# Kernel tuning notes

Measured on AMD Instinct MI355X. Metric: run time of the kernel, lower is better.

The kernel has to match this reference:

```python
import jax, jax.numpy as jnp
from jax import lax
import numpy as np

B, N, D = 32, 256, 4
INF = jnp.float32(1e9)


def cdist(a, b):
    # a: [B,N,D], b: [B,M,D] -> Euclidean cost [B,N,M] (torch.cdist default p=2)
    d = a[:, :, None, :] - b[:, None, :, :]
    return jnp.sqrt(jnp.maximum(jnp.sum(d * d, axis=-1), 0.0))


def hungarian(cost):
    """Exact linear sum assignment (Jonker-Volgenant shortest augmenting path),
    equivalent to scipy.optimize.linear_sum_assignment on a square [n,n] cost.
    Returns col4row[i] = column assigned to row i."""
    n = cost.shape[0]

    def row_step(i, state):  # i in 1..n (1-based row index)
        u, v, p = state  # potentials u:[n+1], v:[n+1]; p[j] = row matched to col j (1-based)
        p = p.at[0].set(i)
        minv = jnp.full(n + 1, INF, dtype=cost.dtype)
        used = jnp.zeros(n + 1, dtype=bool)
        way = jnp.zeros(n + 1, dtype=jnp.int32)
        j0 = jnp.int32(0)

        def cond(c):
            u_, v_, p_, minv_, used_, way_, j0_ = c
            return p_[j0_] != 0

        def body(c):
            u_, v_, p_, minv_, used_, way_, j0_ = c
            used_ = used_.at[j0_].set(True)
            i0 = p_[j0_]
            cur = cost[i0 - 1] - u_[i0] - v_[1:]          # reduced costs for cols 1..n
            cur = jnp.where(used_[1:], INF, cur)
            upd = cur < minv_[1:]
            minv_ = minv_.at[1:].set(jnp.where(upd, cur, minv_[1:]))
            way_ = way_.at[1:].set(jnp.where(upd, j0_, way_[1:]))
            masked = jnp.where(used_[1:], INF, minv_[1:])
            j1 = jnp.argmin(masked).astype(jnp.int32) + 1
            delta = masked[j1 - 1]
            bump = jnp.where(used_, delta, jnp.zeros((), cost.dtype))
            u_ = u_.at[p_].add(bump)                       # u[p[j]] += delta for used j
            v_ = v_ - bump
            minv_ = minv_.at[1:].set(jnp.where(used_[1:], minv_[1:], minv_[1:] - delta))
            return (u_, v_, p_, minv_, used_, way_, j1)

        u, v, p, minv, used, way, j0 = lax.while_loop(cond, body, (u, v, p, minv, used, way, j0))

        def aug_cond(c):
            return c[1] != 0

        def aug_body(c):
            p_, j_ = c
            j1 = way[j_]
            return (p_.at[j_].set(p_[j1]), j1)

        p, _ = lax.while_loop(aug_cond, aug_body, (p, j0))
        return (u, v, p)

    u0 = jnp.zeros(n + 1, dtype=cost.dtype)
    v0 = jnp.zeros(n + 1, dtype=cost.dtype)
    p0 = jnp.zeros(n + 1, dtype=jnp.int32)
    _, _, p = lax.fori_loop(1, n + 1, row_step, (u0, v0, p0))
    # invert: p[j] (1-based row) -> col4row
    col4row = jnp.zeros(n, dtype=jnp.int32).at[p[1:] - 1].set(jnp.arange(n, dtype=jnp.int32))
    return col4row


def setup_inputs() -> dict:
    key = jax.random.key(0)
    k1, k2 = jax.random.split(key)
    pred = jax.random.normal(k1, (B, N, D), dtype=jnp.float32) * 10.0
    gt = jax.random.normal(k2, (B, N, D), dtype=jnp.float32) * 10.0
    return {"pred": pred, "gt": gt}


def reference(pred, gt):
    cost = cdist(pred, gt)                                 # [B,N,N]
    col4row = jax.vmap(hungarian)(cost)                    # [B,N] int32
    matched = jnp.take_along_axis(cost, col4row[:, :, None].astype(jnp.int32), axis=2)[:, :, 0]
    total_cost = matched.sum(axis=-1)                      # [B]
    return col4row, total_cost
```

## Files before the change

kernel.cpp:

```cpp
#include <hip/hip_runtime.h>
#include <math.h>


#define NB   32
#define NN   256
#define ND   4
#define NPT  4
#define INFV 1e9f

#if __has_builtin(__builtin_amdgcn_sqrtf)
__device__ __forceinline__ float fast_sqrtf(float x) { return __builtin_amdgcn_sqrtf(x); }
#else
__device__ __forceinline__ float fast_sqrtf(float x) {
    float r; asm volatile("v_sqrt_f32 %0, %1" : "=v"(r) : "v"(x)); return r;
}
#endif

__device__ __forceinline__ float wave_min_bcast(float x) {
    const int fill = __float_as_int(INFV);
    int a, c;
    a = __builtin_amdgcn_update_dpp(fill, __float_as_int(x), 0x111, 0xF, 0xF, false);
    c = __builtin_amdgcn_update_dpp(fill, __float_as_int(x), 0x112, 0xF, 0xF, false);
    x = fminf(x, fminf(__int_as_float(a), __int_as_float(c)));
    a = __builtin_amdgcn_update_dpp(fill, __float_as_int(x), 0x113, 0xF, 0xF, false);
    c = __builtin_amdgcn_update_dpp(fill, __float_as_int(x), 0x116, 0xF, 0xF, false);
    x = fminf(x, fminf(__int_as_float(a), __int_as_float(c)));
    a = __builtin_amdgcn_update_dpp(fill, __float_as_int(x), 0x117, 0xF, 0xF, false);
    x = fminf(x, __int_as_float(a));
    a = __builtin_amdgcn_update_dpp(fill, __float_as_int(x), 0x142, 0xF, 0xF, false);
    x = fminf(x, __int_as_float(a));
    a = __builtin_amdgcn_update_dpp(fill, __float_as_int(x), 0x143, 0xF, 0xF, false);
    x = fminf(x, __int_as_float(a));
    return __int_as_float(__builtin_amdgcn_readlane(__float_as_int(x), 63));
}

__device__ __forceinline__ float readlane_f(float v, int lane) {
    return __int_as_float(__builtin_amdgcn_readlane(__float_as_int(v), lane));
}
__device__ __forceinline__ int readlane_i(int v, int lane) {
    return __builtin_amdgcn_readlane(v, lane);
}
__device__ __forceinline__ float sel4f(float a0, float a1, float a2, float a3, int kk) {
    float u0 = (kk & 1) ? a1 : a0;
    float u1 = (kk & 1) ? a3 : a2;
    return (kk & 2) ? u1 : u0;
}
__device__ __forceinline__ int sel4i(int a0, int a1, int a2, int a3, int kk) {
    int u0 = (kk & 1) ? a1 : a0;
    int u1 = (kk & 1) ? a3 : a2;
    return (kk & 2) ? u1 : u0;
}

__global__ __launch_bounds__(64) void hungarian_kernel(
    const float* __restrict__ pred, const float* __restrict__ gt,
    float* __restrict__ out)
{
#pragma clang fp contract(off)
    const int b    = blockIdx.x;
    const int lane = threadIdx.x;

    const float* pb = pred + (size_t)b * NN * ND;
    const float* gb = gt   + (size_t)b * NN * ND;

    __shared__ int claimed[NN];

    float gx[NPT], gy[NPT], gz[NPT], gw[NPT];
    float qx[NPT], qy[NPT], qz[NPT], qw[NPT];
    #pragma unroll
    for (int k = 0; k < NPT; ++k) {
        float4 gv = ((const float4*)gb)[4 * lane + k];
        gx[k] = gv.x; gy[k] = gv.y; gz[k] = gv.z; gw[k] = gv.w;
        float4 pv = ((const float4*)pb)[4 * lane + k];
        qx[k] = pv.x; qy[k] = pv.y; qz[k] = pv.z; qw[k] = pv.w;
    }
    float v[NPT], ur[NPT], prx[NPT], pry[NPT], prz[NPT], prw[NPT];
    int pl[NPT];
    #pragma unroll
    for (int k = 0; k < NPT; ++k) {
        v[k] = 0.f; pl[k] = 0; ur[k] = 0.f;
        prx[k] = 0.f; pry[k] = 0.f; prz[k] = 0.f; prw[k] = 0.f;
    }
    const float FINF = __int_as_float(0x7f800000);
    const float NINF = __int_as_float(0xff800000);

    float cmin[NPT];
    int   crow[NPT];
    #pragma unroll
    for (int k = 0; k < NPT; ++k) { cmin[k] = INFV; crow[k] = 0; }
    #pragma unroll 2
    for (int r = 0; r < NN; ++r) {
        const int kkr = r & 3, owr = r >> 2;
        float px = readlane_f(sel4f(qx[0], qx[1], qx[2], qx[3], kkr), owr);
        float py = readlane_f(sel4f(qy[0], qy[1], qy[2], qy[3], kkr), owr);
        float pz = readlane_f(sel4f(qz[0], qz[1], qz[2], qz[3], kkr), owr);
        float pw = readlane_f(sel4f(qw[0], qw[1], qw[2], qw[3], kkr), owr);
        #pragma unroll
        for (int k = 0; k < NPT; ++k) {
            float dx = px - gx[k], dy = py - gy[k];
            float dz = pz - gz[k], dw = pw - gw[k];
            float ss = dx * dx;
            ss = __builtin_fmaf(dy, dy, ss);
            ss = __builtin_fmaf(dz, dz, ss);
            ss = __builtin_fmaf(dw, dw, ss);
            float c = fast_sqrtf(ss);
            bool upd = c < cmin[k];
            crow[k] = upd ? (r + 1) : crow[k];
            cmin[k] = fminf(cmin[k], c);
        }
    }
    #pragma unroll
    for (int k = 0; k < NPT; ++k) claimed[4 * lane + k] = 0x7fffffff;
    __syncthreads();
    #pragma unroll
    for (int k = 0; k < NPT; ++k) atomicMin(&claimed[crow[k] - 1], 4 * lane + k + 1);
    __syncthreads();
    int rm[NPT];
    #pragma unroll
    for (int k = 0; k < NPT; ++k) rm[k] = (claimed[4 * lane + k] != 0x7fffffff);
    #pragma unroll
    for (int k = 0; k < NPT; ++k) {
        v[k]  = cmin[k];
        pl[k] = (claimed[crow[k] - 1] == (4 * lane + k + 1)) ? crow[k] : 0;
    }
    const unsigned long long m0 = __ballot(rm[0]);
    const unsigned long long m1 = __ballot(rm[1]);
    const unsigned long long m2 = __ballot(rm[2]);
    const unsigned long long m3 = __ballot(rm[3]);
    #pragma unroll
    for (int k = 0; k < NPT; ++k) {
        int rr = pl[k];
        if (rr) {
            float4 pv = ((const float4*)pb)[rr - 1];
            prx[k] = pv.x; pry[k] = pv.y; prz[k] = pv.z; prw[k] = pv.w;
        }
    }

    for (int i = 1; i <= NN; ++i) {
        const int im1 = i - 1;
        const unsigned long long mm = (im1 & 2) ? ((im1 & 1) ? m3 : m2)
                                                : ((im1 & 1) ? m1 : m0);
        if ((mm >> (im1 >> 2)) & 1ull) continue;

        const int kki = im1 & 3, owi = im1 >> 2;
        float4 pr0;
        pr0.x = readlane_f(sel4f(qx[0], qx[1], qx[2], qx[3], kki), owi);
        pr0.y = readlane_f(sel4f(qy[0], qy[1], qy[2], qy[3], kki), owi);
        pr0.z = readlane_f(sel4f(qz[0], qz[1], qz[2], qz[3], kki), owi);
        pr0.w = readlane_f(sel4f(qw[0], qw[1], qw[2], qw[3], kki), owi);
        float4 pr = pr0;

        int codes[NPT];
        #pragma unroll
        for (int k = 0; k < NPT; ++k) codes[k] = (4 * lane + k + 1) | (pl[k] << 12);
        float minv[NPT], vm[NPT], ucol[NPT], mcol[NPT];
        int   wayr[NPT];
        #pragma unroll
        for (int k = 0; k < NPT; ++k) {
            minv[k] = INFV; vm[k] = v[k]; ucol[k] = 0.f; mcol[k] = 0.f; wayr[k] = 0;
        }
        float u_i = 0.f;
        int   j1  = 0;
        float ui  = 0.f;
        int   i0n = i;

        for (int it = 0; it < NN + 2; ++it) {
            const int   jm1 = j1 - 1;
            const float bu  = ui - u_i;
            #pragma unroll
            for (int k = 0; k < NPT; ++k) {
                bool hit = (4 * lane + k) == jm1;
                vm[k]   = hit ? NINF : vm[k];
                minv[k] = hit ? FINF : minv[k];
                ucol[k] = hit ? bu   : ucol[k];
                mcol[k] = hit ? u_i  : mcol[k];
            }
            #pragma unroll
            for (int k = 0; k < NPT; ++k) {
                float dx = pr.x - gx[k], dy = pr.y - gy[k];
                float dz = pr.z - gz[k], dw = pr.w - gw[k];
                float ss = dx * dx;
                ss = __builtin_fmaf(dy, dy, ss);
                ss = __builtin_fmaf(dz, dz, ss);
                ss = __builtin_fmaf(dw, dw, ss);
                float cur = (fast_sqrtf(ss) - ui) - vm[k];
                bool upd = cur < minv[k];
                wayr[k] = upd ? j1 : wayr[k];
                minv[k] = fminf(minv[k], cur);
            }
            bool s01 = minv[1] < minv[0];
            float v01 = s01 ? minv[1] : minv[0];
            int   c01 = s01 ? codes[1] : codes[0];
            float u01 = s01 ? ur[1] : ur[0];
            float x01 = s01 ? prx[1] : prx[0];
            float y01 = s01 ? pry[1] : pry[0];
            float z01 = s01 ? prz[1] : prz[0];
            float w01 = s01 ? prw[1] : prw[0];
            bool s23 = minv[3] < minv[2];
            float v23 = s23 ? minv[3] : minv[2];
            int   c23 = s23 ? codes[3] : codes[2];
            float u23 = s23 ? ur[3] : ur[2];
            float x23 = s23 ? prx[3] : prx[2];
            float y23 = s23 ? pry[3] : pry[2];
            float z23 = s23 ? prz[3] : prz[2];
            float w23 = s23 ? prw[3] : prw[2];
            bool sF  = v23 < v01;
            float best       = sF ? v23 : v01;
            int   code_local = sF ? c23 : c01;
            float usel = sF ? u23 : u01;
            float xsel = sF ? x23 : x01;
            float ysel = sF ? y23 : y01;
            float zsel = sF ? z23 : z01;
            float wsel = sF ? w23 : w01;
            const float gmin = wave_min_bcast(best);
            unsigned long long msk = __ballot(best == gmin);
            int owner = __ffsll(msk) - 1;
            int code  = readlane_i(code_local, owner);
            int j1n   = code & 0xFFF;
            i0n       = code >> 12;
            const float delta = gmin;
            #pragma unroll
            for (int k = 0; k < NPT; ++k) minv[k] -= delta;
            u_i += delta;
            j1 = j1n;
            if (i0n == 0) break;
            ui   = readlane_f(usel, owner);
            pr.x = readlane_f(xsel, owner);
            pr.y = readlane_f(ysel, owner);
            pr.z = readlane_f(zsel, owner);
            pr.w = readlane_f(wsel, owner);
        }

        #pragma unroll
        for (int k = 0; k < NPT; ++k) {
            bool used = (minv[k] == FINF);
            float un = ucol[k] + u_i;
            ur[k] = used ? un : ur[k];
            v[k]  = used ? ((v[k] - u_i) + mcol[k]) : v[k];
        }
        int j = j1;
        while (j != 0) {
            int kj = (j - 1) & 3, oj = (j - 1) >> 2;
            int jp = readlane_i(sel4i(wayr[0], wayr[1], wayr[2], wayr[3], kj), oj);
            bool z = (jp == 0);
            int kp = z ? 0 : ((jp - 1) & 3);
            int op = z ? 0 : ((jp - 1) >> 2);
            int   val  = readlane_i(sel4i(pl[0], pl[1], pl[2], pl[3], kp), op);
            float unew = readlane_f(sel4f(ur[0], ur[1], ur[2], ur[3], kp), op);
            float pnx  = readlane_f(sel4f(prx[0], prx[1], prx[2], prx[3], kp), op);
            float pny  = readlane_f(sel4f(pry[0], pry[1], pry[2], pry[3], kp), op);
            float pnz  = readlane_f(sel4f(prz[0], prz[1], prz[2], prz[3], kp), op);
            float pnw  = readlane_f(sel4f(prw[0], prw[1], prw[2], prw[3], kp), op);
            val  = z ? i     : val;
            unew = z ? u_i   : unew;
            pnx  = z ? pr0.x : pnx;
            pny  = z ? pr0.y : pny;
            pnz  = z ? pr0.z : pnz;
            pnw  = z ? pr0.w : pnw;
            #pragma unroll
            for (int k = 0; k < NPT; ++k) {
                bool hit = (4 * lane + k) == (j - 1);
                pl[k]  = hit ? val  : pl[k];
                ur[k]  = hit ? unew : ur[k];
                prx[k] = hit ? pnx  : prx[k];
                pry[k] = hit ? pny  : pry[k];
                prz[k] = hit ? pnz  : prz[k];
                prw[k] = hit ? pnw  : prw[k];
            }
            j = jp;
        }
    }

    float tot = 0.f;
    #pragma unroll
    for (int k = 0; k < NPT; ++k) {
        int j = 4 * lane + k;
        int r = pl[k];
        out[b * NN + (r - 1)] = (float)j;
        float dx = prx[k] - gx[k], dy = pry[k] - gy[k];
        float dz = prz[k] - gz[k], dw = prw[k] - gw[k];
        tot += sqrtf(dx * dx + dy * dy + dz * dz + dw * dw);
    }
    for (int off = 32; off; off >>= 1) tot += __shfl_xor(tot, off);
    if (lane == 0) out[NB * NN + b] = tot;
}

extern "C" void kernel_launch(void* const* d_in, const int* in_sizes, int n_in,
                              void* d_out, int out_size, void* d_ws, size_t ws_size,
                              hipStream_t stream) {
    const float* pred = (const float*)d_in[0];
    const float* gt   = (const float*)d_in[1];
    float* out = (float*)d_out;
    hipLaunchKernelGGL(hungarian_kernel, dim3(NB), dim3(64), 0, stream,
                       pred, gt, out);
}
```

Measured before the change: 1.478 ms.

## Add augmenting row reduction passes before shortest-path phase in Hungarian kernel

Inserts a JV-style augmenting row reduction phase after column reduction. Each free row finds its best and second-best reduced costs through wave-wide min reductions, takes its best column, lowers that column's potential, and may displace the column's previous owner, with a cap of 768 events. Rows left free are then handled by the existing shortest augmenting path loop, which now iterates over a free-row mask instead of a matched mask. The aim is to leave far fewer rows for the expensive per-row Dijkstra searches, at the cost of extra serial wave reductions and a risk to exact optimality or tie-breaking agreement with the reference.

Measured after the change: 1.623 ms. 9.9% more time.

```diff
diff --git a/kernel.cpp b/kernel.cpp
--- a/kernel.cpp
+++ b/kernel.cpp
@@ -122,10 +122,10 @@
         v[k]  = cmin[k];
         pl[k] = (claimed[crow[k] - 1] == (4 * lane + k + 1)) ? crow[k] : 0;
     }
-    const unsigned long long m0 = __ballot(rm[0]);
-    const unsigned long long m1 = __ballot(rm[1]);
-    const unsigned long long m2 = __ballot(rm[2]);
-    const unsigned long long m3 = __ballot(rm[3]);
+    unsigned long long fm0 = ~__ballot(rm[0]);
+    unsigned long long fm1 = ~__ballot(rm[1]);
+    unsigned long long fm2 = ~__ballot(rm[2]);
+    unsigned long long fm3 = ~__ballot(rm[3]);
     #pragma unroll
     for (int k = 0; k < NPT; ++k) {
         int rr = pl[k];
@@ -135,11 +135,119 @@
         }
     }
 
+    {
+        int events = 0;
+        for (int pass = 0; pass < 2; ++pass) {
+            for (int r = 1; r <= NN; ++r) {
+                const int rmm = r - 1;
+                const unsigned long long fsel =
+                    (rmm & 2) ? ((rmm & 1) ? fm3 : fm2)
+                              : ((rmm & 1) ? fm1 : fm0);
+                if (!((fsel >> (rmm >> 2)) & 1ull)) continue;
+                int i = r;
+                for (;;) {
+                    if (++events > 768) break;
+                    const int im1 = i - 1, ki = im1 & 3, li = im1 >> 2;
+                    float px = readlane_f(sel4f(qx[0], qx[1], qx[2], qx[3], ki), li);
+                    float py = readlane_f(sel4f(qy[0], qy[1], qy[2], qy[3], ki), li);
+                    float pz = readlane_f(sel4f(qz[0], qz[1], qz[2], qz[3], ki), li);
+                    float pw = readlane_f(sel4f(qw[0], qw[1], qw[2], qw[3], ki), li);
+                    float rr[NPT];
+                    #pragma unroll
+                    for (int k = 0; k < NPT; ++k) {
+                        float dx = px - gx[k], dy = py - gy[k];
+                        float dz = pz - gz[k], dw = pw - gw[k];
+                        float ss = dx * dx;
+                        ss = __builtin_fmaf(dy, dy, ss);
+                        ss = __builtin_fmaf(dz, dz, ss);
+                        ss = __builtin_fmaf(dw, dw, ss);
+                        rr[k] = fast_sqrtf(ss) - v[k];
+                    }
+                    bool s01 = rr[1] < rr[0];
+                    float a1 = s01 ? rr[1] : rr[0];
+                    int   ac = s01 ? (4 * lane + 2) : (4 * lane + 1);
+                    bool s23 = rr[3] < rr[2];
+                    float b1 = s23 ? rr[3] : rr[2];
+                    int   bc = s23 ? (4 * lane + 4) : (4 * lane + 3);
+                    bool sF = b1 < a1;
+                    float l1 = sF ? b1 : a1;
+                    int   lc = sF ? bc : ac;
+                    const float u1 = wave_min_bcast(l1);
+                    unsigned long long msk1 = __ballot(l1 == u1);
+                    int own1 = __ffsll(msk1) - 1;
+                    int j1 = readlane_i(lc, own1);
+                    const int jm1 = j1 - 1;
+                    float rs[NPT];
+                    #pragma unroll
+                    for (int k = 0; k < NPT; ++k)
+                        rs[k] = ((4 * lane + k) == jm1) ? FINF : rr[k];
+                    bool t01 = rs[1] < rs[0];
+                    float c1 = t01 ? rs[1] : rs[0];
+                    int   cc = t01 ? (4 * lane + 2) : (4 * lane + 1);
+                    bool t23 = rs[3] < rs[2];
+                    float d1 = t23 ? rs[3] : rs[2];
+                    int   dc = t23 ? (4 * lane + 4) : (4 * lane + 3);
+                    bool tF = d1 < c1;
+                    float l2 = tF ? d1 : c1;
+                    int   lc2 = tF ? dc : cc;
+                    const float u2 = wave_min_bcast(l2);
+                    unsigned long long msk2 = __ballot(l2 == u2);
+                    int own2 = __ffsll(msk2) - 1;
+                    int j2 = readlane_i(lc2, own2);
+                    int i0a = readlane_i(sel4i(pl[0], pl[1], pl[2], pl[3], jm1 & 3), jm1 >> 2);
+                    const bool strict = u1 < u2;
+                    int jm, inew;
+                    if (strict) {
+                        jm = j1; inew = i0a;
+                    } else if (i0a != 0) {
+                        jm = j2;
+                        const int j2m1 = j2 - 1;
+                        inew = readlane_i(sel4i(pl[0], pl[1], pl[2], pl[3], j2m1 & 3), j2m1 >> 2);
+                    } else {
+                        jm = j1; inew = 0;
+                    }
+                    const float vdec = strict ? (u2 - u1) : 0.f;
+                    const int jmm1 = jm - 1;
+                    #pragma unroll
+                    for (int k = 0; k < NPT; ++k) {
+                        bool hit = (4 * lane + k) == jmm1;
+                        v[k]   = hit ? (v[k] - vdec) : v[k];
+                        pl[k]  = hit ? i   : pl[k];
+                        ur[k]  = hit ? u2  : ur[k];
+                        prx[k] = hit ? px  : prx[k];
+                        pry[k] = hit ? py  : pry[k];
+                        prz[k] = hit ? pz  : prz[k];
+                        prw[k] = hit ? pw  : prw[k];
+                    }
+                    {
+                        const unsigned long long bi = 1ull << li;
+                        fm0 = (ki == 0) ? (fm0 & ~bi) : fm0;
+                        fm1 = (ki == 1) ? (fm1 & ~bi) : fm1;
+                        fm2 = (ki == 2) ? (fm2 & ~bi) : fm2;
+                        fm3 = (ki == 3) ? (fm3 & ~bi) : fm3;
+                    }
+                    if (inew == 0) break;
+                    {
+                        const int nm1 = inew - 1, kn = nm1 & 3;
+                        const unsigned long long bn = 1ull << (nm1 >> 2);
+                        fm0 = (kn == 0) ? (fm0 | bn) : fm0;
+                        fm1 = (kn == 1) ? (fm1 | bn) : fm1;
+                        fm2 = (kn == 2) ? (fm2 | bn) : fm2;
+                        fm3 = (kn == 3) ? (fm3 | bn) : fm3;
+                    }
+                    if (!strict) break;
+                    i = inew;
+                }
+            }
+        }
+    }
+
+
     for (int i = 1; i <= NN; ++i) {
         const int im1 = i - 1;
-        const unsigned long long mm = (im1 & 2) ? ((im1 & 1) ? m3 : m2)
-                                                : ((im1 & 1) ? m1 : m0);
-        if ((mm >> (im1 >> 2)) & 1ull) continue;
+        const unsigned long long mm = (im1 & 2) ? ((im1 & 1) ? fm3 : fm2)
+                                                : ((im1 & 1) ? fm1 : fm0);
+        if (!((mm >> (im1 >> 2)) & 1ull)) continue;
 
         const int kki = im1 & 3, owi = im1 >> 2;
         float4 pr0;
```

## Add auction-style augmenting row reduction before shortest-path phase

Applied to the files above, without the earlier changes.

Adds a bounded loop of parallel augmenting-row-reduction rounds, as in Jonker-Volgenant. Each free row finds its best and second-best reduced cost, bids for its best column, and on winning updates the column potential and displaces the previous owner. This cuts the number of rows left for the serial shortest augmenting path loop. In exchange it adds several rounds of full 256-column scans, extra LDS state and syncs, and it only handles up to 64 free rows per round.

Result: faster. 1.200 ms, median of 2 (-18.8%).

```diff
diff --git a/kernel.cpp b/kernel.cpp
--- a/kernel.cpp
+++ b/kernel.cpp
@@ -7,6 +7,7 @@
 #define ND   4
 #define NPT  4
 #define INFV 1e9f
+#define MAXR 12
 
 #if __has_builtin(__builtin_amdgcn_sqrtf)
 __device__ __forceinline__ float fast_sqrtf(float x) { return __builtin_amdgcn_sqrtf(x); }
@@ -62,7 +63,13 @@
     const float* pb = pred + (size_t)b * NN * ND;
     const float* gb = gt   + (size_t)b * NN * ND;
 
-    __shared__ int claimed[NN];
+    __shared__ int   claimed[NN];
+    __shared__ int   free_lds[NN];
+    __shared__ int   list_lds[NN];
+    __shared__ int   mb_row[NN];
+    __shared__ float mb_u2[NN], mb_d[NN];
+    __shared__ float mb_px[NN], mb_py[NN], mb_pz[NN], mb_pw[NN];
+    __shared__ int   cnt_lds;
 
     float gx[NPT], gy[NPT], gz[NPT], gw[NPT];
     float qx[NPT], qy[NPT], qz[NPT], qw[NPT];
@@ -122,10 +129,8 @@
         v[k]  = cmin[k];
         pl[k] = (claimed[crow[k] - 1] == (4 * lane + k + 1)) ? crow[k] : 0;
     }
-    const unsigned long long m0 = __ballot(rm[0]);
-    const unsigned long long m1 = __ballot(rm[1]);
-    const unsigned long long m2 = __ballot(rm[2]);
-    const unsigned long long m3 = __ballot(rm[3]);
+    #pragma unroll
+    for (int k = 0; k < NPT; ++k) free_lds[4 * lane + k] = rm[k] ? 0 : 1;
     #pragma unroll
     for (int k = 0; k < NPT; ++k) {
         int rr = pl[k];
@@ -135,11 +140,94 @@
         }
     }
 
+    {
+        int prevF = 0x7fffffff, stall = 0;
+        for (int round = 0; round < MAXR; ++round) {
+            if (lane == 0) cnt_lds = 0;
+            __syncthreads();
+            #pragma unroll
+            for (int k = 0; k < NPT; ++k) {
+                int r4 = 4 * lane + k;
+                mb_row[r4] = 0x7fffffff;
+                if (free_lds[r4]) {
+                    int s = atomicAdd(&cnt_lds, 1);
+                    list_lds[s] = r4 + 1;
+                }
+            }
+            __syncthreads();
+            const int F = cnt_lds;
+            if (F == 0) break;
+            if (F >= prevF) { if (++stall >= 3) break; } else stall = 0;
+            prevF = F;
+
+            const bool act = lane < F;
+            const int  row = act ? list_lds[lane] : 1;
+            float4 pv = ((const float4*)pb)[row - 1];
+            float m1 = INFV, m2 = INFV;
+            int   j1c = 1;
+            for (int ow = 0; ow < 64; ++ow) {
+                #pragma unroll
+                for (int kk = 0; kk < NPT; ++kk) {
+                    float cgx = readlane_f(gx[kk], ow);
+                    float cgy = readlane_f(gy[kk], ow);
+                    float cgz = readlane_f(gz[kk], ow);
+                    float cgw = readlane_f(gw[kk], ow);
+                    float cvv = readlane_f(v[kk],  ow);
+                    float dx = pv.x - cgx, dy = pv.y - cgy;
+                    float dz = pv.z - cgz, dw = pv.w - cgw;
+                    float ss = dx * dx;
+                    ss = __builtin_fmaf(dy, dy, ss);
+                    ss = __builtin_fmaf(dz, dz, ss);
+                    ss = __builtin_fmaf(dw, dw, ss);
+                    float c = fast_sqrtf(ss) - cvv;
+                    bool lt = c < m1;
+                    m2  = lt ? m1 : fminf(m2, c);
+                    j1c = lt ? (4 * ow + kk + 1) : j1c;
+                    m1  = lt ? c : m1;
+                }
+            }
+            if (act) atomicMin(&mb_row[j1c - 1], row);
+            __syncthreads();
+            const bool won = act && (mb_row[j1c - 1] == row);
+            if (won) {
+                mb_u2[j1c - 1] = m2;
+                mb_d [j1c - 1] = m2 - m1;
+                mb_px[j1c - 1] = pv.x; mb_py[j1c - 1] = pv.y;
+                mb_pz[j1c - 1] = pv.z; mb_pw[j1c - 1] = pv.w;
+            }
+            __syncthreads();
+            #pragma unroll
+            for (int k = 0; k < NPT; ++k) {
+                const int c4 = 4 * lane + k;
+                const int wr = mb_row[c4];
+                if (wr != 0x7fffffff) {
+                    const int old = pl[k];
+                    if (old) free_lds[old - 1] = 1;
+                    free_lds[wr - 1] = 0;
+                    pl[k]  = wr;
+                    ur[k]  = mb_u2[c4];
+                    v[k]  -= mb_d[c4];
+                    prx[k] = mb_px[c4]; pry[k] = mb_py[c4];
+                    prz[k] = mb_pz[c4]; prw[k] = mb_pw[c4];
+                }
+            }
+        }
+    }
+    __syncthreads();
+    int fr[NPT];
+    #pragma unroll
+    for (int k = 0; k < NPT; ++k) fr[k] = free_lds[4 * lane + k];
+    const unsigned long long fm0 = __ballot(fr[0] != 0);
+    const unsigned long long fm1 = __ballot(fr[1] != 0);
+    const unsigned long long fm2 = __ballot(fr[2] != 0);
+    const unsigned long long fm3 = __ballot(fr[3] != 0);
+
+
     for (int i = 1; i <= NN; ++i) {
         const int im1 = i - 1;
-        const unsigned long long mm = (im1 & 2) ? ((im1 & 1) ? m3 : m2)
-                                                : ((im1 & 1) ? m1 : m0);
-        if ((mm >> (im1 >> 2)) & 1ull) continue;
+        const unsigned long long mm = (im1 & 2) ? ((im1 & 1) ? fm3 : fm2)
+                                                : ((im1 & 1) ? fm1 : fm0);
+        if (!((mm >> (im1 >> 2)) & 1ull)) continue;
 
         const int kki = im1 & 3, owi = im1 >> 2;
         float4 pr0;
```
